# Optimization experiments

Hardware: AMD Instinct MI355X
Metric: run time of the kernel (lower is better)

The kernel has to match this reference:

```python
import jax, jax.numpy as jnp
import numpy as np

IN_F = 4096
OUT_F = 4096
RANK = 16
ALPHA = 32.0


def setup_inputs() -> dict:
    key = jax.random.key(0)
    k1, k2, k3, k4, k5 = jax.random.split(key, 5)
    x = jax.random.normal(k1, (4, 2048, IN_F), dtype=jnp.float32)
    W = jax.random.normal(k2, (OUT_F, IN_F), dtype=jnp.float32) * (1.0 / np.sqrt(IN_F))
    b = jax.random.normal(k3, (OUT_F,), dtype=jnp.float32) * 0.01
    # torch init: lora_A ~ uniform(0.01, 1.0) per nn.init.uniform_(a=0.01); lora_B zeros.
    # Use nonzero B here so the adapter path is numerically exercised.
    lora_A = jax.random.uniform(k4, (RANK, IN_F), dtype=jnp.float32, minval=0.01, maxval=1.0)
    lora_B = jax.random.normal(k5, (OUT_F, RANK), dtype=jnp.float32) * 0.01
    return {"x": x, "W": W, "b": b, "lora_A": lora_A, "lora_B": lora_B}


def reference(x, W, b, lora_A, lora_B):
    scaling = ALPHA / RANK
    # base linear: x @ W.T + b   -> [B, S, out]
    base = jnp.einsum("bsi,oi->bso", x, W) + b
    # low-rank adapter: (x @ A.T) @ B.T * scaling
    xa = jnp.einsum("bsi,ri->bsr", x, lora_A)        # [B, S, rank]
    adj = jnp.einsum("bsr,or->bso", xa, lora_B) * scaling
    return base + adj
```

## Files before the change

### kernel.cpp

```cpp
#include <hip/hip_runtime.h>
#include <hip/hip_bf16.h>
#include <stdint.h>

#define MM 8192
#define NN 4096
#define KK 4096
#define RANK 16
#define SCALING 2.0f

typedef __bf16 bf16x8 __attribute__((ext_vector_type(8)));
typedef float  f32x4  __attribute__((ext_vector_type(4)));

__device__ inline void async_copy16(const void* g, void* lds) {
    __builtin_amdgcn_global_load_lds(
        (const __attribute__((address_space(1))) void*)g,
        (__attribute__((address_space(3))) void*)lds,
        16, 0, 0);
}

#define CONV_BLOCKS 16384

__global__ __launch_bounds__(256, 8)
void conv_x_kernel(const float* __restrict__ x, __hip_bfloat16* __restrict__ xb) {
    size_t i = (size_t)blockIdx.x * 256 + threadIdx.x;
    const float4* s = (const float4*)x + i * 2;
    float4 a = s[0], b = s[1];
    union { __hip_bfloat16 h[8]; uint4 u; } o;
    o.h[0] = __float2bfloat16(a.x); o.h[1] = __float2bfloat16(a.y);
    o.h[2] = __float2bfloat16(a.z); o.h[3] = __float2bfloat16(a.w);
    o.h[4] = __float2bfloat16(b.x); o.h[5] = __float2bfloat16(b.y);
    o.h[6] = __float2bfloat16(b.z); o.h[7] = __float2bfloat16(b.w);
    *((uint4*)xb + i) = o.u;
}

#define PREP_BLOCKS 8192

__global__ __launch_bounds__(256, 4)
void prep_w_kernel(const float* __restrict__ W,
                   const float* __restrict__ lA,
                   const float* __restrict__ lB,
                   __hip_bfloat16* __restrict__ wb) {
    size_t idx = (size_t)blockIdx.x * 256 + threadIdx.x;
    int o  = (int)(idx >> 9);
    int i0 = ((int)idx & 511) << 3;
    const float4* wp = (const float4*)(W + (size_t)o * KK + i0);
    float4 w0 = wp[0], w1 = wp[1];
    const float4* bp = (const float4*)(lB + (size_t)o * RANK);
    float4 bq0 = bp[0], bq1 = bp[1], bq2 = bp[2], bq3 = bp[3];
    float bv[RANK] = { bq0.x, bq0.y, bq0.z, bq0.w,
                       bq1.x, bq1.y, bq1.z, bq1.w,
                       bq2.x, bq2.y, bq2.z, bq2.w,
                       bq3.x, bq3.y, bq3.z, bq3.w };
    float acc[8] = {0,0,0,0,0,0,0,0};
#pragma unroll 4
    for (int r = 0; r < RANK; ++r) {
        float b = bv[r];
        const float4* ap = (const float4*)(lA + (size_t)r * KK + i0);
        float4 a0 = ap[0], a1 = ap[1];
        acc[0] += b * a0.x; acc[1] += b * a0.y;
        acc[2] += b * a0.z; acc[3] += b * a0.w;
        acc[4] += b * a1.x; acc[5] += b * a1.y;
        acc[6] += b * a1.z; acc[7] += b * a1.w;
    }
    float res[8] = { w0.x + SCALING * acc[0], w0.y + SCALING * acc[1],
                     w0.z + SCALING * acc[2], w0.w + SCALING * acc[3],
                     w1.x + SCALING * acc[4], w1.y + SCALING * acc[5],
                     w1.z + SCALING * acc[6], w1.w + SCALING * acc[7] };
    union { __hip_bfloat16 h[8]; uint4 u; } pk;
#pragma unroll
    for (int j = 0; j < 8; ++j) pk.h[j] = __float2bfloat16(res[j]);
    *((uint4*)wb + idx) = pk.u;
}

#define BM 128
#define BN 128
#define BK 64

__global__ __launch_bounds__(256, 3)
void gemm_bt_kernel(const __hip_bfloat16* __restrict__ A,
                    const __hip_bfloat16* __restrict__ B,
                    const float* __restrict__ bias,
                    float* __restrict__ C) {
    __shared__ __align__(16) __hip_bfloat16 As[BM * BK];
    __shared__ __align__(16) __hip_bfloat16 Bs[BN * BK];

    const int t     = threadIdx.x;
    const int lane  = t & 63;
    const int wave  = t >> 6;
    const int wm    = wave >> 1;
    const int wn    = wave & 1;
    const int row16 = lane & 15;
    const int quad  = lane >> 4;
    const int bm = blockIdx.y, bn = blockIdx.x;

    f32x4 acc[4][4] = {};

    const int srow   = t >> 3;
    const int schunk = ((t & 7) ^ ((t >> 3) & 7)) * 8;
    const __hip_bfloat16* gA = A + (size_t)(bm * BM + srow) * KK + schunk;
    const __hip_bfloat16* gB = B + (size_t)(bn * BN + srow) * KK + schunk;

    char* ldsA = (char*)As + wave * 1024;
    char* ldsB = (char*)Bs + wave * 1024;

    for (int kt = 0; kt < KK; kt += BK) {
#pragma unroll
        for (int s = 0; s < 4; ++s) {
            async_copy16(gA + (size_t)(32 * s) * KK + kt, ldsA + s * 4096);
            async_copy16(gB + (size_t)(32 * s) * KK + kt, ldsB + s * 4096);
        }
        __syncthreads();

#pragma unroll
        for (int h = 0; h < 2; ++h) {
            bf16x8 af[4], bg[4];
            const int cbase = 4 * h + quad;
            const int slot  = (cbase ^ (row16 & 7)) * 8;
#pragma unroll
            for (int mi = 0; mi < 4; ++mi)
                af[mi] = *(const bf16x8*)(As + (wm * 64 + mi * 16 + row16) * BK + slot);
#pragma unroll
            for (int ni = 0; ni < 4; ++ni)
                bg[ni] = *(const bf16x8*)(Bs + (wn * 64 + ni * 16 + row16) * BK + slot);
#pragma unroll
            for (int mi = 0; mi < 4; ++mi)
#pragma unroll
                for (int ni = 0; ni < 4; ++ni)
                    acc[mi][ni] = __builtin_amdgcn_mfma_f32_16x16x32_bf16(
                        af[mi], bg[ni], acc[mi][ni], 0, 0, 0);
        }
        __syncthreads();
    }

    const int colBase = bn * BN + wn * 64;
    const int rowBase = bm * BM + wm * 64;
#pragma unroll
    for (int ni = 0; ni < 4; ++ni) {
        int col = colBase + ni * 16 + row16;
        float bv = bias[col];
#pragma unroll
        for (int mi = 0; mi < 4; ++mi) {
            int r0 = rowBase + mi * 16 + quad * 4;
#pragma unroll
            for (int i = 0; i < 4; ++i)
                C[(size_t)(r0 + i) * NN + col] = acc[mi][ni][i] + bv;
        }
    }
}

__global__ void naive_base_kernel(const float* __restrict__ x,
                                  const float* __restrict__ W,
                                  const float* __restrict__ b,
                                  float* __restrict__ out) {
    size_t idx = (size_t)blockIdx.x * 256 + threadIdx.x;
    int m = (int)(idx / NN), n = (int)(idx % NN);
    const float* xr = x + (size_t)m * KK;
    const float* wr = W + (size_t)n * KK;
    float s = 0.f;
    for (int k = 0; k < KK; ++k) s += xr[k] * wr[k];
    out[idx] = s + b[n];
}

__global__ void naive_adapter_kernel(const float* __restrict__ x,
                                     const float* __restrict__ lA,
                                     const float* __restrict__ lB,
                                     float* __restrict__ out) {
    int m = blockIdx.x;
    __shared__ float xa[RANK];
    __shared__ float red[256];
    const float* xr = x + (size_t)m * KK;
    for (int r = 0; r < RANK; ++r) {
        float p = 0.f;
        for (int k = threadIdx.x; k < KK; k += 256) p += xr[k] * lA[(size_t)r * KK + k];
        red[threadIdx.x] = p;
        __syncthreads();
        for (int s = 128; s > 0; s >>= 1) {
            if (threadIdx.x < s) red[threadIdx.x] += red[threadIdx.x + s];
            __syncthreads();
        }
        if (threadIdx.x == 0) xa[r] = red[0];
        __syncthreads();
    }
    for (int n = threadIdx.x; n < NN; n += 256) {
        float adj = 0.f;
#pragma unroll
        for (int r = 0; r < RANK; ++r) adj += xa[r] * lB[n * RANK + r];
        out[(size_t)m * NN + n] += SCALING * adj;
    }
}

extern "C" void kernel_launch(void* const* d_in, const int* in_sizes, int n_in,
                              void* d_out, int out_size, void* d_ws, size_t ws_size,
                              hipStream_t stream) {
    const float* x  = (const float*)d_in[0];
    const float* W  = (const float*)d_in[1];
    const float* b  = (const float*)d_in[2];
    const float* lA = (const float*)d_in[3];
    const float* lB = (const float*)d_in[4];
    float* out = (float*)d_out;

    size_t need = (size_t)MM * KK * 2 + (size_t)NN * KK * 2;
    if (ws_size >= need) {
        __hip_bfloat16* xb = (__hip_bfloat16*)d_ws;
        __hip_bfloat16* wb = xb + (size_t)MM * KK;
        conv_x_kernel<<<CONV_BLOCKS, 256, 0, stream>>>(x, xb);
        prep_w_kernel<<<PREP_BLOCKS, 256, 0, stream>>>(W, lA, lB, wb);
        gemm_bt_kernel<<<dim3(NN / BN, MM / BM), 256, 0, stream>>>(xb, wb, b, out);
    } else {
        naive_base_kernel<<<(size_t)MM * NN / 256, 256, 0, stream>>>(x, W, b, out);
        naive_adapter_kernel<<<MM, 256, 0, stream>>>(x, lA, lB, out);
    }
}
```

Measured before the change: 567.0 us.

## Replace GEMM with 256x256 double-buffered, barrier-scheduled 8-wave kernel

```diff
diff --git a/kernel.cpp b/kernel.cpp
--- a/kernel.cpp
+++ b/kernel.cpp
@@ -11,12 +11,14 @@
 typedef __bf16 bf16x8 __attribute__((ext_vector_type(8)));
 typedef float  f32x4  __attribute__((ext_vector_type(4)));
 
-__device__ inline void async_copy16(const void* g, void* lds) {
+__device__ __forceinline__ void async_copy16(const void* g, void* lds) {
     __builtin_amdgcn_global_load_lds(
         (const __attribute__((address_space(1))) void*)g,
         (__attribute__((address_space(3))) void*)lds,
         16, 0, 0);
 }
+
+#define CFENCE asm volatile("" ::: "memory")
 
 #define CONV_BLOCKS 16384
 
@@ -72,78 +74,159 @@
     *((uint4*)wb + idx) = pk.u;
 }
 
-#define BM 128
-#define BN 128
-#define BK 64
-
-__global__ __launch_bounds__(256, 3)
-void gemm_bt_kernel(const __hip_bfloat16* __restrict__ A,
+#define GBM 256
+#define GBN 256
+#define GBK 64
+#define NT (KK / GBK)
+
+__device__ __forceinline__ void ldsA4(bf16x8 (&a)[4][2], const __hip_bfloat16* as,
+                                      int rowbase, int slot0, int slot1) {
+#pragma unroll
+    for (int mi = 0; mi < 4; ++mi) {
+        const __hip_bfloat16* p = as + (size_t)(rowbase + mi * 16) * 64;
+        a[mi][0] = *(const bf16x8*)(p + slot0);
+        a[mi][1] = *(const bf16x8*)(p + slot1);
+    }
+}
+
+__device__ __forceinline__ void ldsB2(bf16x8 (&b)[2][2], const __hip_bfloat16* bs,
+                                      int rowbase, int slot0, int slot1) {
+#pragma unroll
+    for (int ni = 0; ni < 2; ++ni) {
+        const __hip_bfloat16* p = bs + (size_t)(rowbase + ni * 16) * 64;
+        b[ni][0] = *(const bf16x8*)(p + slot0);
+        b[ni][1] = *(const bf16x8*)(p + slot1);
+    }
+}
+
+__device__ __forceinline__ void mfma_quad(f32x4 (&acc)[8][4], const bf16x8 (&a)[4][2],
+                                          const bf16x8 (&b)[2][2], int mg0, int ng0) {
+#pragma unroll
+    for (int mi = 0; mi < 4; ++mi)
+#pragma unroll
+        for (int ni = 0; ni < 2; ++ni)
+#pragma unroll
+            for (int h = 0; h < 2; ++h)
+                acc[mg0 + mi][ng0 + ni] = __builtin_amdgcn_mfma_f32_16x16x32_bf16(
+                    a[mi][h], b[ni][h], acc[mg0 + mi][ng0 + ni], 0, 0, 0);
+}
+
+__global__ __launch_bounds__(512, 2)
+void gemm256_kernel(const __hip_bfloat16* __restrict__ A,
                     const __hip_bfloat16* __restrict__ B,
                     const float* __restrict__ bias,
                     float* __restrict__ C) {
-    __shared__ __align__(16) __hip_bfloat16 As[BM * BK];
-    __shared__ __align__(16) __hip_bfloat16 Bs[BN * BK];
+    __shared__ __align__(16) __hip_bfloat16 As[2][GBM * GBK];
+    __shared__ __align__(16) __hip_bfloat16 Bs[2][GBN * GBK];
 
     const int t     = threadIdx.x;
     const int lane  = t & 63;
     const int wave  = t >> 6;
-    const int wm    = wave >> 1;
-    const int wn    = wave & 1;
+    const int wm    = wave >> 2;
+    const int wn    = wave & 3;
     const int row16 = lane & 15;
     const int quad  = lane >> 4;
-    const int bm = blockIdx.y, bn = blockIdx.x;
-
-    f32x4 acc[4][4] = {};
-
-    const int srow   = t >> 3;
-    const int schunk = ((t & 7) ^ ((t >> 3) & 7)) * 8;
-    const __hip_bfloat16* gA = A + (size_t)(bm * BM + srow) * KK + schunk;
-    const __hip_bfloat16* gB = B + (size_t)(bn * BN + srow) * KK + schunk;
-
-    char* ldsA = (char*)As + wave * 1024;
-    char* ldsB = (char*)Bs + wave * 1024;
-
-    for (int kt = 0; kt < KK; kt += BK) {
-#pragma unroll
-        for (int s = 0; s < 4; ++s) {
-            async_copy16(gA + (size_t)(32 * s) * KK + kt, ldsA + s * 4096);
-            async_copy16(gB + (size_t)(32 * s) * KK + kt, ldsB + s * 4096);
-        }
-        __syncthreads();
-
-#pragma unroll
-        for (int h = 0; h < 2; ++h) {
-            bf16x8 af[4], bg[4];
-            const int cbase = 4 * h + quad;
-            const int slot  = (cbase ^ (row16 & 7)) * 8;
-#pragma unroll
-            for (int mi = 0; mi < 4; ++mi)
-                af[mi] = *(const bf16x8*)(As + (wm * 64 + mi * 16 + row16) * BK + slot);
-#pragma unroll
-            for (int ni = 0; ni < 4; ++ni)
-                bg[ni] = *(const bf16x8*)(Bs + (wn * 64 + ni * 16 + row16) * BK + slot);
-#pragma unroll
-            for (int mi = 0; mi < 4; ++mi)
-#pragma unroll
-                for (int ni = 0; ni < 4; ++ni)
-                    acc[mi][ni] = __builtin_amdgcn_mfma_f32_16x16x32_bf16(
-                        af[mi], bg[ni], acc[mi][ni], 0, 0, 0);
-        }
-        __syncthreads();
-    }
-
-    const int colBase = bn * BN + wn * 64;
-    const int rowBase = bm * BM + wm * 64;
-#pragma unroll
-    for (int ni = 0; ni < 4; ++ni) {
-        int col = colBase + ni * 16 + row16;
+
+    const int bid = blockIdx.x;
+    const int swz = (bid & 7) * 64 + (bid >> 3);
+    const int bm  = swz >> 4;
+    const int bn  = swz & 15;
+
+    const int ssub   = lane >> 3;
+    const int schunk = ((lane & 7) ^ ssub) * 8;
+    const int awave  = wave * 8;
+    const int bwave  = (wave & 3) * 8 + (wave >> 2) * 64;
+
+    const __hip_bfloat16* gA = A + (size_t)(bm * GBM) * KK;
+    const __hip_bfloat16* gB = B + (size_t)(bn * GBN) * KK;
+
+#define STG_A(buf, rb, kt) \
+    async_copy16(gA + (size_t)((rb) + awave + ssub) * KK + (kt) + schunk, \
+                 (char*)(As[buf]) + ((rb) + awave) * 128)
+#define STG_B(buf, rb, kt) \
+    async_copy16(gB + (size_t)((rb) + bwave + ssub) * KK + (kt) + schunk, \
+                 (char*)(Bs[buf]) + ((rb) + bwave) * 128)
+
+    f32x4 acc[8][4] = {};
+
+    const int slot0 = (quad ^ (row16 & 7)) * 8;
+    const int slot1 = slot0 ^ 32;
+
+    STG_A(0, 0, 0);    STG_A(0, 128, 0);
+    STG_B(0, 0, 0);    STG_B(0, 128, 0);
+    STG_A(0, 64, 0);   STG_A(0, 192, 0);
+    STG_B(0, 32, 0);   STG_B(0, 160, 0);
+    CFENCE;
+    STG_A(1, 0, GBK);  STG_A(1, 128, GBK);
+    STG_B(1, 0, GBK);  STG_B(1, 128, GBK);
+    STG_A(1, 64, GBK); STG_A(1, 192, GBK);
+    asm volatile("s_waitcnt vmcnt(6)" ::: "memory");
+    CFENCE; __builtin_amdgcn_s_barrier(); CFENCE;
+
+    for (int tk = 0; tk < NT; ++tk) {
+        const int cur = tk & 1, nxt = cur ^ 1;
+        const __hip_bfloat16* as = As[cur];
+        const __hip_bfloat16* bs = Bs[cur];
+        const int kt1 = (tk + 1) * GBK;
+        const int kt2 = (tk + 2) * GBK;
+        const bool s0  = tk < NT - 1;
+        const bool s12 = tk < NT - 2;
+
+        bf16x8 af[4][2], b0[2][2], b1[2][2];
+
+        ldsA4(af, as, wm * 128 + row16, slot0, slot1);
+        ldsB2(b0, bs, wn * 64 + row16, slot0, slot1);
+        if (s0) { STG_B(nxt, 32, kt1); STG_B(nxt, 160, kt1); }
+        CFENCE; __builtin_amdgcn_s_barrier();
+        asm volatile("s_waitcnt lgkmcnt(0)" ::: "memory");
+        __builtin_amdgcn_s_setprio(1);
+        mfma_quad(acc, af, b0, 0, 0);
+        __builtin_amdgcn_s_setprio(0);
+        CFENCE; __builtin_amdgcn_s_barrier(); CFENCE;
+
+        ldsB2(b1, bs, wn * 64 + 32 + row16, slot0, slot1);
+        if (s12) { STG_A(cur, 0, kt2); STG_A(cur, 128, kt2); }
+        CFENCE; __builtin_amdgcn_s_barrier();
+        asm volatile("s_waitcnt lgkmcnt(0)" ::: "memory");
+        __builtin_amdgcn_s_setprio(1);
+        mfma_quad(acc, af, b1, 0, 2);
+        __builtin_amdgcn_s_setprio(0);
+        CFENCE; __builtin_amdgcn_s_barrier(); CFENCE;
+
+        ldsA4(af, as, wm * 128 + 64 + row16, slot0, slot1);
+        if (s12) { STG_B(cur, 0, kt2); STG_B(cur, 128, kt2); }
+        CFENCE; __builtin_amdgcn_s_barrier();
+        asm volatile("s_waitcnt lgkmcnt(0)" ::: "memory");
+        __builtin_amdgcn_s_setprio(1);
+        mfma_quad(acc, af, b1, 4, 2);
+        __builtin_amdgcn_s_setprio(0);
+        CFENCE; __builtin_amdgcn_s_barrier(); CFENCE;
+
+        if (s12) { STG_A(cur, 64, kt2); STG_A(cur, 192, kt2); }
+        CFENCE; __builtin_amdgcn_s_barrier();
+        asm volatile("s_waitcnt lgkmcnt(0)" ::: "memory");
+        __builtin_amdgcn_s_setprio(1);
+        mfma_quad(acc, af, b0, 4, 0);
+        __builtin_amdgcn_s_setprio(0);
+        if (s12) asm volatile("s_waitcnt vmcnt(6)" ::: "memory");
+        else     asm volatile("s_waitcnt vmcnt(0)" ::: "memory");
+        CFENCE; __builtin_amdgcn_s_barrier(); CFENCE;
+    }
+#undef STG_A
+#undef STG_B
+
+    const int colBase = bn * GBN + wn * 64;
+    const int rowBase = bm * GBM + wm * 128;
+#pragma unroll
+    for (int ng = 0; ng < 4; ++ng) {
+        int col = colBase + ng * 16 + row16;
         float bv = bias[col];
 #pragma unroll
-        for (int mi = 0; mi < 4; ++mi) {
-            int r0 = rowBase + mi * 16 + quad * 4;
+        for (int mg = 0; mg < 8; ++mg) {
+            int r0 = rowBase + mg * 16 + quad * 4;
 #pragma unroll
             for (int i = 0; i < 4; ++i)
-                C[(size_t)(r0 + i) * NN + col] = acc[mi][ni][i] + bv;
+                C[(size_t)(r0 + i) * NN + col] = acc[mg][ng][i] + bv;
         }
     }
 }
@@ -205,7 +288,7 @@
         __hip_bfloat16* wb = xb + (size_t)MM * KK;
         conv_x_kernel<<<CONV_BLOCKS, 256, 0, stream>>>(x, xb);
         prep_w_kernel<<<PREP_BLOCKS, 256, 0, stream>>>(W, lA, lB, wb);
-        gemm_bt_kernel<<<dim3(NN / BN, MM / BM), 256, 0, stream>>>(xb, wb, b, out);
+        gemm256_kernel<<<(MM / GBM) * (NN / GBN), 512, 0, stream>>>(xb, wb, b, out);
     } else {
         naive_base_kernel<<<(size_t)MM * NN / 256, 256, 0, stream>>>(x, W, b, out);
         naive_adapter_kernel<<<MM, 256, 0, stream>>>(x, lA, lB, out);
```

Measured after the change: 618.1 us. 1.09x slower.

## Fuse fp32-to-bf16 conversion of x into the GEMM A-tile load

Applied to the files above, without the earlier changes.

```diff
diff --git a/kernel.cpp b/kernel.cpp
--- a/kernel.cpp
+++ b/kernel.cpp
@@ -11,26 +11,11 @@
 typedef __bf16 bf16x8 __attribute__((ext_vector_type(8)));
 typedef float  f32x4  __attribute__((ext_vector_type(4)));
 
-__device__ inline void async_copy16(const void* g, void* lds) {
+__device__ __forceinline__ void async_copy16(const void* g, void* lds) {
     __builtin_amdgcn_global_load_lds(
         (const __attribute__((address_space(1))) void*)g,
         (__attribute__((address_space(3))) void*)lds,
         16, 0, 0);
-}
-
-#define CONV_BLOCKS 16384
-
-__global__ __launch_bounds__(256, 8)
-void conv_x_kernel(const float* __restrict__ x, __hip_bfloat16* __restrict__ xb) {
-    size_t i = (size_t)blockIdx.x * 256 + threadIdx.x;
-    const float4* s = (const float4*)x + i * 2;
-    float4 a = s[0], b = s[1];
-    union { __hip_bfloat16 h[8]; uint4 u; } o;
-    o.h[0] = __float2bfloat16(a.x); o.h[1] = __float2bfloat16(a.y);
-    o.h[2] = __float2bfloat16(a.z); o.h[3] = __float2bfloat16(a.w);
-    o.h[4] = __float2bfloat16(b.x); o.h[5] = __float2bfloat16(b.y);
-    o.h[6] = __float2bfloat16(b.z); o.h[7] = __float2bfloat16(b.w);
-    *((uint4*)xb + i) = o.u;
 }
 
 #define PREP_BLOCKS 8192
@@ -77,10 +62,10 @@
 #define BK 64
 
 __global__ __launch_bounds__(256, 3)
-void gemm_bt_kernel(const __hip_bfloat16* __restrict__ A,
-                    const __hip_bfloat16* __restrict__ B,
-                    const float* __restrict__ bias,
-                    float* __restrict__ C) {
+void gemm_xf32_kernel(const float* __restrict__ X,
+                      const __hip_bfloat16* __restrict__ B,
+                      const float* __restrict__ bias,
+                      float* __restrict__ C) {
     __shared__ __align__(16) __hip_bfloat16 As[BM * BK];
     __shared__ __align__(16) __hip_bfloat16 Bs[BN * BK];
 
@@ -96,18 +81,32 @@
     f32x4 acc[4][4] = {};
 
     const int srow   = t >> 3;
-    const int schunk = ((t & 7) ^ ((t >> 3) & 7)) * 8;
-    const __hip_bfloat16* gA = A + (size_t)(bm * BM + srow) * KK + schunk;
-    const __hip_bfloat16* gB = B + (size_t)(bn * BN + srow) * KK + schunk;
-
-    char* ldsA = (char*)As + wave * 1024;
+    const int chunkA = (t & 7) * 8;
+    const int slotA  = ((t & 7) ^ (srow & 7)) * 8;
+    const int schunkB = slotA;
+    const float* gX = X + (size_t)(bm * BM + srow) * KK + chunkA;
+    const __hip_bfloat16* gB = B + (size_t)(bn * BN + srow) * KK + schunkB;
+
     char* ldsB = (char*)Bs + wave * 1024;
 
     for (int kt = 0; kt < KK; kt += BK) {
+        float4 fa[4], fb[4];
 #pragma unroll
         for (int s = 0; s < 4; ++s) {
-            async_copy16(gA + (size_t)(32 * s) * KK + kt, ldsA + s * 4096);
+            const float4* p = (const float4*)(gX + (size_t)(32 * s) * KK + kt);
+            fa[s] = p[0]; fb[s] = p[1];
+        }
+#pragma unroll
+        for (int s = 0; s < 4; ++s)
             async_copy16(gB + (size_t)(32 * s) * KK + kt, ldsB + s * 4096);
+#pragma unroll
+        for (int s = 0; s < 4; ++s) {
+            union { __hip_bfloat16 h[8]; uint4 u; } pk;
+            pk.h[0] = __float2bfloat16(fa[s].x); pk.h[1] = __float2bfloat16(fa[s].y);
+            pk.h[2] = __float2bfloat16(fa[s].z); pk.h[3] = __float2bfloat16(fa[s].w);
+            pk.h[4] = __float2bfloat16(fb[s].x); pk.h[5] = __float2bfloat16(fb[s].y);
+            pk.h[6] = __float2bfloat16(fb[s].z); pk.h[7] = __float2bfloat16(fb[s].w);
+            *(uint4*)(As + (size_t)(srow + 32 * s) * BK + slotA) = pk.u;
         }
         __syncthreads();
 
@@ -199,13 +198,11 @@
     const float* lB = (const float*)d_in[4];
     float* out = (float*)d_out;
 
-    size_t need = (size_t)MM * KK * 2 + (size_t)NN * KK * 2;
+    size_t need = (size_t)NN * KK * 2;
     if (ws_size >= need) {
-        __hip_bfloat16* xb = (__hip_bfloat16*)d_ws;
-        __hip_bfloat16* wb = xb + (size_t)MM * KK;
-        conv_x_kernel<<<CONV_BLOCKS, 256, 0, stream>>>(x, xb);
+        __hip_bfloat16* wb = (__hip_bfloat16*)d_ws;
         prep_w_kernel<<<PREP_BLOCKS, 256, 0, stream>>>(W, lA, lB, wb);
-        gemm_bt_kernel<<<dim3(NN / BN, MM / BM), 256, 0, stream>>>(xb, wb, b, out);
+        gemm_xf32_kernel<<<dim3(NN / BN, MM / BM), 256, 0, stream>>>(x, wb, b, out);
     } else {
         naive_base_kernel<<<(size_t)MM * NN / 256, 256, 0, stream>>>(x, W, b, out);
         naive_adapter_kernel<<<MM, 256, 0, stream>>>(x, lA, lB, out);
```

Result: slower. 626.7 us (+10.5%).
